# Kernel optimization log

Hardware: AMD Instinct MI355X
Metric: run time of the kernel (lower is better)

The kernel has to match this reference:

```python
import jax, jax.numpy as jnp
import numpy as np

B, C, T, F = 4, 2, 4224, 256
L = 256          # sequence_len (block size over time)
STRIDE = 128
H = 8            # num_heads
RF = L // 2      # receptive_field default


def setup_inputs() -> dict:
    key = jax.random.key(0)
    k0, k1, k2, k3, k4 = jax.random.split(key, 5)
    s = 0.05
    return {
        "x": jax.random.normal(k0, (B, C, T, F), dtype=jnp.float32),
        "w_in": jax.random.normal(k1, (3 * F, F), dtype=jnp.float32) * s,
        "b_in": jax.random.normal(k2, (3 * F,), dtype=jnp.float32) * s,
        "w_out": jax.random.normal(k3, (F, F), dtype=jnp.float32) * s,
        "b_out": jax.random.normal(k4, (F,), dtype=jnp.float32) * s,
    }


def reference(x, w_in, b_in, w_out, b_out):
    b, c, t, f = x.shape
    nb = (t - L) // STRIDE + 1              # num_blocks
    dh = f // H                              # head dim

    # --- UnfoldSpectrogram: (B,C,T,F) -> (B,C,nb,L,F) ---
    idx = jnp.arange(nb)[:, None] * STRIDE + jnp.arange(L)[None, :]  # (nb, L)
    blocks = x[:, :, idx, :]                 # (B,C,nb,L,F)

    # --- MultiheadAttention over flattened batch of blocks ---
    xb = blocks.reshape(b * c * nb, L, f)    # (N,L,F)
    qkv = xb @ w_in.T + b_in                 # (N,L,3F)
    q, k, v = jnp.split(qkv, 3, axis=-1)
    q = q.reshape(-1, L, H, dh)
    k = k.reshape(-1, L, H, dh)
    v = v.reshape(-1, L, H, dh)

    scale = 1.0 / np.sqrt(dh).astype(np.float32)
    scores = jnp.einsum("nihd,njhd->nhij", q, k) * scale  # (N,H,L,L)

    # Faithful to the original: the Longformer mask is a FLOAT 0/1 tensor that
    # torch's MultiheadAttention ADDS to the scores (band gets +1.0).
    di = jnp.arange(L)[:, None] - jnp.arange(L)[None, :]
    band = ((di >= 0) & (di < RF)).astype(scores.dtype)   # (L,L)
    scores = scores + band

    attn = jax.nn.softmax(scores, axis=-1)
    o = jnp.einsum("nhij,njhd->nihd", attn, v).reshape(-1, L, f)
    o = o @ w_out.T + b_out                  # (N,L,F)

    # --- FoldSpectrogram: overlap-add then normalize by overlap count ---
    ob = o.reshape(b, c, nb, L, f)
    y = jnp.zeros((b, c, t, f), dtype=o.dtype).at[:, :, idx, :].add(ob)
    cnt = jnp.zeros((t,), dtype=o.dtype).at[idx.reshape(-1)].add(1.0)
    return y / cnt[None, None, :, None]
```

## Files before the change

### kernel.cpp

```cpp
#include <hip/hip_runtime.h>

typedef unsigned short u16;
typedef unsigned int u32;
typedef __attribute__((ext_vector_type(8))) short bf16x8;
typedef __attribute__((ext_vector_type(4))) float f32x4;
typedef __attribute__((ext_vector_type(4))) u32 u32x4;
typedef __attribute__((ext_vector_type(2))) u32 u32x2;

__device__ __forceinline__ u16 f2bf(float f) {
  u32 u = __builtin_bit_cast(u32, f);
  return (u16)((u + 0x7FFFu + ((u >> 16) & 1u)) >> 16);
}
__device__ __forceinline__ float bf2f(u16 b) {
  return __builtin_bit_cast(float, (u32)b << 16);
}

__device__ __forceinline__ void lds_async16(const void* g, void* l) {
  auto gp = reinterpret_cast<const __attribute__((address_space(1))) u32*>(
      reinterpret_cast<uintptr_t>(g));
  auto lp = reinterpret_cast<__attribute__((address_space(3))) u32*>(
      reinterpret_cast<uintptr_t>(l));
  __builtin_amdgcn_global_load_lds(gp, lp, 16, 0, 0);
}

__global__ void cvt_kernel(const float* __restrict__ in, u16* __restrict__ out, int n4) {
  int i = blockIdx.x * 256 + threadIdx.x;
  if (i < n4) {
    f32x4 v = *(const f32x4*)(in + (size_t)i * 4);
    u32x2 o;
    o[0] = (u32)f2bf(v[0]) | ((u32)f2bf(v[1]) << 16);
    o[1] = (u32)f2bf(v[2]) | ((u32)f2bf(v[3]) << 16);
    *(u32x2*)(out + (size_t)i * 4) = o;
  }
}

template <bool OUT_BF16>
__global__ __launch_bounds__(256) void gemm_bt_kernel(
    const u16* __restrict__ A, const u16* __restrict__ B,
    const float* __restrict__ bias, void* __restrict__ C,
    int M, int N, int K) {
  __shared__ u16 sA[128 * 32];
  __shared__ u16 sB[128 * 32];
  const int tid = threadIdx.x;
  const int m0 = blockIdx.x * 128;
  const int n0 = blockIdx.y * 128;
  const int w = tid >> 6;
  const int lane = tid & 63;
  const int wr = (w >> 1) * 64;
  const int wc = (w & 1) * 64;
  const int lm = lane & 15;
  const int lk = (lane >> 4) * 8;

  f32x4 acc[4][4] = {};

  const int srow = tid >> 2;
  const int ssub = (tid & 3) * 8;
  const u16* Ag = A + (size_t)(m0 + srow) * K + ssub;
  const u16* Bg = B + (size_t)(n0 + srow) * K + ssub;
  const size_t rstep = (size_t)64 * K;

  for (int k0 = 0; k0 < K; k0 += 32) {
    __syncthreads();
    lds_async16(Ag + k0, &sA[tid * 8]);
    lds_async16(Ag + rstep + k0, &sA[2048 + tid * 8]);
    lds_async16(Bg + k0, &sB[tid * 8]);
    lds_async16(Bg + rstep + k0, &sB[2048 + tid * 8]);
    __syncthreads();
    bf16x8 af[4], bfr[4];
#pragma unroll
    for (int i = 0; i < 4; ++i)
      af[i] = *(const bf16x8*)&sA[(wr + i * 16 + lm) * 32 + lk];
#pragma unroll
    for (int j = 0; j < 4; ++j)
      bfr[j] = *(const bf16x8*)&sB[(wc + j * 16 + lm) * 32 + lk];
#pragma unroll
    for (int i = 0; i < 4; ++i)
#pragma unroll
      for (int j = 0; j < 4; ++j)
        acc[i][j] = __builtin_amdgcn_mfma_f32_16x16x32_bf16(af[i], bfr[j], acc[i][j], 0, 0, 0);
  }

  const int r0 = (lane >> 4) * 4;
#pragma unroll
  for (int j = 0; j < 4; ++j) {
    const int n = n0 + wc + j * 16 + lm;
    const float bv = bias[n];
#pragma unroll
    for (int i = 0; i < 4; ++i) {
#pragma unroll
      for (int r = 0; r < 4; ++r) {
        const int m = m0 + wr + i * 16 + r0 + r;
        float v = acc[i][j][r] + bv;
        if (OUT_BF16)
          ((u16*)C)[(size_t)m * N + n] = f2bf(v);
        else
          ((float*)C)[(size_t)m * N + n] = v;
      }
    }
  }
}

__global__ __launch_bounds__(256, 2) void attn_kernel(const u16* __restrict__ qkv,
                                                      u16* __restrict__ o_ws) {
  __shared__ u16 sK[256 * 40];
  __shared__ u16 sVt[32 * 264];
  __shared__ u16 sP[4 * 64 * 72];

  const int bid = blockIdx.x;
  const int n = bid >> 3;
  const int h = bid & 7;
  const int rowbase = (n >> 5) * 4224 + (n & 31) * 128;
  const int tid = threadIdx.x;
  const int w = tid >> 6;
  const int lane = tid & 63;
  const int lm = lane & 15;
  const int lg = lane >> 4;

#pragma unroll
  for (int it = 0; it < 4; ++it) {
    int c = it * 256 + tid;
    int row = c >> 2;
    int sub = (c & 3) * 8;
    const u16* gk = qkv + (size_t)(rowbase + row) * 768 + 256 + h * 32 + sub;
    *(u32x4*)&sK[row * 40 + sub] = *(const u32x4*)gk;
    const u16* gv = qkv + (size_t)(rowbase + row) * 768 + 512 + h * 32 + sub;
    u32x4 vv = *(const u32x4*)gv;
#pragma unroll
    for (int q = 0; q < 4; ++q) {
      sVt[(sub + 2 * q) * 264 + row] = (u16)(vv[q] & 0xFFFFu);
      sVt[(sub + 2 * q + 1) * 264 + row] = (u16)(vv[q] >> 16);
    }
  }

  bf16x8 qf[4];
#pragma unroll
  for (int rt = 0; rt < 4; ++rt) {
    int row = rowbase + w * 64 + rt * 16 + lm;
    qf[rt] = *(const bf16x8*)(qkv + (size_t)row * 768 + h * 32 + lg * 8);
  }

  __syncthreads();

  f32x4 oacc[4][2] = {};
  float lsum[4][4] = {};
  u16* myP = sP + w * (64 * 72);
  const float scale = 0.17677669529663687f;

  for (int ch = 0; ch < 4; ++ch) {
    bf16x8 kf[4];
#pragma unroll
    for (int ct = 0; ct < 4; ++ct)
      kf[ct] = *(const bf16x8*)&sK[(ch * 64 + ct * 16 + lm) * 40 + lg * 8];
    f32x4 s[4][4] = {};
#pragma unroll
    for (int rt = 0; rt < 4; ++rt)
#pragma unroll
      for (int ct = 0; ct < 4; ++ct)
        s[rt][ct] = __builtin_amdgcn_mfma_f32_16x16x32_bf16(qf[rt], kf[ct], s[rt][ct], 0, 0, 0);

#pragma unroll
    for (int rt = 0; rt < 4; ++rt)
#pragma unroll
      for (int ct = 0; ct < 4; ++ct) {
        int j = ch * 64 + ct * 16 + lm;
#pragma unroll
        for (int r = 0; r < 4; ++r) {
          int i = w * 64 + rt * 16 + lg * 4 + r;
          int di = i - j;
          float sv = s[rt][ct][r] * scale + ((di >= 0 && di < 128) ? 1.0f : 0.0f);
          float p = __expf(sv);
          lsum[rt][r] += p;
          myP[(rt * 16 + lg * 4 + r) * 72 + ct * 16 + lm] = f2bf(p);
        }
      }

#pragma unroll
    for (int kt = 0; kt < 2; ++kt) {
      bf16x8 pf[4], vf[2];
#pragma unroll
      for (int rt = 0; rt < 4; ++rt)
        pf[rt] = *(const bf16x8*)&myP[(rt * 16 + lm) * 72 + kt * 32 + lg * 8];
#pragma unroll
      for (int ct = 0; ct < 2; ++ct)
        vf[ct] = *(const bf16x8*)&sVt[(ct * 16 + lm) * 264 + ch * 64 + kt * 32 + lg * 8];
#pragma unroll
      for (int rt = 0; rt < 4; ++rt)
#pragma unroll
        for (int ct = 0; ct < 2; ++ct)
          oacc[rt][ct] = __builtin_amdgcn_mfma_f32_16x16x32_bf16(pf[rt], vf[ct], oacc[rt][ct], 0, 0, 0);
    }
  }

#pragma unroll
  for (int rt = 0; rt < 4; ++rt)
#pragma unroll
    for (int r = 0; r < 4; ++r) {
      float v = lsum[rt][r];
      v += __shfl_xor(v, 1);
      v += __shfl_xor(v, 2);
      v += __shfl_xor(v, 4);
      v += __shfl_xor(v, 8);
      lsum[rt][r] = 1.0f / v;
    }

#pragma unroll
  for (int rt = 0; rt < 4; ++rt)
#pragma unroll
    for (int ct = 0; ct < 2; ++ct)
#pragma unroll
      for (int r = 0; r < 4; ++r) {
        int i = w * 64 + rt * 16 + lg * 4 + r;
        int d = ct * 16 + lm;
        float v = oacc[rt][ct][r] * lsum[rt][r];
        o_ws[((size_t)(n * 256 + i)) * 256 + h * 32 + d] = f2bf(v);
      }
}

__global__ void combine_kernel(const u16* __restrict__ o_ws, u16* __restrict__ oc) {
  int gid = blockIdx.x * 256 + threadIdx.x;
  int m = gid >> 5;
  int f0 = (gid & 31) << 3;
  int bc = m / 4224;
  int t = m - bc * 4224;
  int i0 = t >> 7;
  float a[8] = {0.f, 0.f, 0.f, 0.f, 0.f, 0.f, 0.f, 0.f};
  if (i0 <= 31) {
    const u16* p = o_ws + ((size_t)((bc * 32 + i0) * 256 + (t - (i0 << 7)))) * 256 + f0;
    u32x4 v = *(const u32x4*)p;
#pragma unroll
    for (int q = 0; q < 4; ++q) {
      a[2 * q] += bf2f((u16)(v[q] & 0xFFFFu));
      a[2 * q + 1] += bf2f((u16)(v[q] >> 16));
    }
  }
  if (i0 >= 1) {
    int i1 = i0 - 1;
    const u16* p = o_ws + ((size_t)((bc * 32 + i1) * 256 + (t - (i1 << 7)))) * 256 + f0;
    u32x4 v = *(const u32x4*)p;
#pragma unroll
    for (int q = 0; q < 4; ++q) {
      a[2 * q] += bf2f((u16)(v[q] & 0xFFFFu));
      a[2 * q + 1] += bf2f((u16)(v[q] >> 16));
    }
  }
  float sc = (i0 >= 1 && i0 <= 31) ? 0.5f : 1.0f;
  u32x2 o;
  o[0] = (u32)f2bf(a[0] * sc) | ((u32)f2bf(a[1] * sc) << 16);
  o[1] = (u32)f2bf(a[2] * sc) | ((u32)f2bf(a[3] * sc) << 16);
  u32x2 o2;
  o2[0] = (u32)f2bf(a[4] * sc) | ((u32)f2bf(a[5] * sc) << 16);
  o2[1] = (u32)f2bf(a[6] * sc) | ((u32)f2bf(a[7] * sc) << 16);
  u16* dst = oc + (size_t)m * 256 + f0;
  *(u32x2*)dst = o;
  *(u32x2*)(dst + 4) = o2;
}

extern "C" void kernel_launch(void* const* d_in, const int* in_sizes, int n_in,
                              void* d_out, int out_size, void* d_ws, size_t ws_size,
                              hipStream_t stream) {
  const float* x = (const float*)d_in[0];
  const float* w_in = (const float*)d_in[1];
  const float* b_in = (const float*)d_in[2];
  const float* w_out = (const float*)d_in[3];
  const float* b_out = (const float*)d_in[4];
  float* y = (float*)d_out;
  char* ws = (char*)d_ws;

  u16* qkv = (u16*)(ws);
  u16* xbf = (u16*)(ws + 51904512);
  u16* ows = (u16*)(ws + 69206016);
  u16* winb = (u16*)(ws + 102760448);
  u16* woutb = (u16*)(ws + 103153664);

  cvt_kernel<<<8448, 256, 0, stream>>>(x, xbf, 2162688);
  cvt_kernel<<<192, 256, 0, stream>>>(w_in, winb, 49152);
  cvt_kernel<<<64, 256, 0, stream>>>(w_out, woutb, 16384);

  gemm_bt_kernel<true><<<dim3(264, 6), 256, 0, stream>>>(xbf, winb, b_in, qkv, 33792, 768, 256);

  attn_kernel<<<2048, 256, 0, stream>>>(qkv, ows);

  combine_kernel<<<4224, 256, 0, stream>>>(ows, xbf);

  gemm_bt_kernel<false><<<dim3(264, 2), 256, 0, stream>>>(xbf, woutb, b_out, y, 33792, 256, 256);
}
```

Before: 202.6 us.

## Restructure attention kernel: transposed scores, direct K loads, exp2 softmax, higher occupancy

Result: slower. 395.2 us (+95.1%).

```diff
diff --git a/kernel.cpp b/kernel.cpp
--- a/kernel.cpp
+++ b/kernel.cpp
@@ -13,6 +13,14 @@
 }
 __device__ __forceinline__ float bf2f(u16 b) {
   return __builtin_bit_cast(float, (u32)b << 16);
+}
+
+__device__ __forceinline__ float fexp2(float x) {
+#if __has_builtin(__builtin_amdgcn_exp2f)
+  return __builtin_amdgcn_exp2f(x);
+#else
+  return __expf(x * 0.6931471805599453f);
+#endif
 }
 
 __device__ __forceinline__ void lds_async16(const void* g, void* l) {
@@ -100,11 +108,10 @@
   }
 }
 
-__global__ __launch_bounds__(256, 2) void attn_kernel(const u16* __restrict__ qkv,
+__global__ __launch_bounds__(256, 4) void attn_kernel(const u16* __restrict__ qkv,
                                                       u16* __restrict__ o_ws) {
-  __shared__ u16 sK[256 * 40];
   __shared__ u16 sVt[32 * 264];
-  __shared__ u16 sP[4 * 64 * 72];
+  __shared__ u16 sP[4 * 64 * 40];
 
   const int bid = blockIdx.x;
   const int n = bid >> 3;
@@ -121,8 +128,6 @@
     int c = it * 256 + tid;
     int row = c >> 2;
     int sub = (c & 3) * 8;
-    const u16* gk = qkv + (size_t)(rowbase + row) * 768 + 256 + h * 32 + sub;
-    *(u32x4*)&sK[row * 40 + sub] = *(const u32x4*)gk;
     const u16* gv = qkv + (size_t)(rowbase + row) * 768 + 512 + h * 32 + sub;
     u32x4 vv = *(const u32x4*)gv;
 #pragma unroll
@@ -142,78 +147,103 @@
   __syncthreads();
 
   f32x4 oacc[4][2] = {};
-  float lsum[4][4] = {};
-  u16* myP = sP + w * (64 * 72);
-  const float scale = 0.17677669529663687f;
-
-  for (int ch = 0; ch < 4; ++ch) {
-    bf16x8 kf[4];
-#pragma unroll
-    for (int ct = 0; ct < 4; ++ct)
-      kf[ct] = *(const bf16x8*)&sK[(ch * 64 + ct * 16 + lm) * 40 + lg * 8];
-    f32x4 s[4][4] = {};
+  float lsum[4] = {0.f, 0.f, 0.f, 0.f};
+  u16* myP = sP + w * (64 * 40);
+  const float C1 = 0.25500035370494726f;
+  const float C2 = 1.4426950408889634f;
+  const int jq = lg * 4;
+
+  for (int ch = 0; ch < 8; ++ch) {
+    bf16x8 kf[2];
+#pragma unroll
+    for (int ct = 0; ct < 2; ++ct)
+      kf[ct] = *(const bf16x8*)(qkv +
+          (size_t)(rowbase + ch * 32 + ct * 16 + lm) * 768 + 256 + h * 32 + lg * 8);
+
+    f32x4 st[2][4] = {};
+#pragma unroll
+    for (int ct = 0; ct < 2; ++ct)
+#pragma unroll
+      for (int rt = 0; rt < 4; ++rt)
+        st[ct][rt] = __builtin_amdgcn_mfma_f32_16x16x32_bf16(kf[ct], qf[rt], st[ct][rt], 0, 0, 0);
+
+#pragma unroll
+    for (int ct = 0; ct < 2; ++ct) {
+#pragma unroll
+      for (int rt = 0; rt < 4; ++rt) {
+        const int D0 = w * 64 + rt * 16 - (ch * 32 + ct * 16);
+        f32x4 s = st[ct][rt];
+        float p0, p1, p2, p3;
+        if (D0 >= 16 && D0 <= 112) {
+          p0 = fexp2(__builtin_fmaf(s[0], C1, C2));
+          p1 = fexp2(__builtin_fmaf(s[1], C1, C2));
+          p2 = fexp2(__builtin_fmaf(s[2], C1, C2));
+          p3 = fexp2(__builtin_fmaf(s[3], C1, C2));
+        } else if (D0 == 0) {
+          p0 = fexp2(__builtin_fmaf(s[0], C1, (lm >= jq + 0) ? C2 : 0.0f));
+          p1 = fexp2(__builtin_fmaf(s[1], C1, (lm >= jq + 1) ? C2 : 0.0f));
+          p2 = fexp2(__builtin_fmaf(s[2], C1, (lm >= jq + 2) ? C2 : 0.0f));
+          p3 = fexp2(__builtin_fmaf(s[3], C1, (lm >= jq + 3) ? C2 : 0.0f));
+        } else if (D0 == 128) {
+          p0 = fexp2(__builtin_fmaf(s[0], C1, (lm < jq + 0) ? C2 : 0.0f));
+          p1 = fexp2(__builtin_fmaf(s[1], C1, (lm < jq + 1) ? C2 : 0.0f));
+          p2 = fexp2(__builtin_fmaf(s[2], C1, (lm < jq + 2) ? C2 : 0.0f));
+          p3 = fexp2(__builtin_fmaf(s[3], C1, (lm < jq + 3) ? C2 : 0.0f));
+        } else {
+          p0 = fexp2(s[0] * C1);
+          p1 = fexp2(s[1] * C1);
+          p2 = fexp2(s[2] * C1);
+          p3 = fexp2(s[3] * C1);
+        }
+        lsum[rt] += (p0 + p1) + (p2 + p3);
+        u32 u0 = __builtin_bit_cast(u32, p0) + 0x8000u;
+        u32 u1 = __builtin_bit_cast(u32, p1) + 0x8000u;
+        u32 u2 = __builtin_bit_cast(u32, p2) + 0x8000u;
+        u32 u3 = __builtin_bit_cast(u32, p3) + 0x8000u;
+        u32x2 pk;
+        pk[0] = __builtin_amdgcn_perm(u1, u0, 0x07060302u);
+        pk[1] = __builtin_amdgcn_perm(u3, u2, 0x07060302u);
+        *(u32x2*)&myP[(rt * 16 + lm) * 40 + ct * 16 + jq] = pk;
+      }
+    }
+
+    bf16x8 pf[4], vf[2];
 #pragma unroll
     for (int rt = 0; rt < 4; ++rt)
-#pragma unroll
-      for (int ct = 0; ct < 4; ++ct)
-        s[rt][ct] = __builtin_amdgcn_mfma_f32_16x16x32_bf16(qf[rt], kf[ct], s[rt][ct], 0, 0, 0);
-
+      pf[rt] = *(const bf16x8*)&myP[(rt * 16 + lm) * 40 + lg * 8];
+#pragma unroll
+    for (int ctd = 0; ctd < 2; ++ctd)
+      vf[ctd] = *(const bf16x8*)&sVt[(ctd * 16 + lm) * 264 + ch * 32 + lg * 8];
 #pragma unroll
     for (int rt = 0; rt < 4; ++rt)
 #pragma unroll
-      for (int ct = 0; ct < 4; ++ct) {
-        int j = ch * 64 + ct * 16 + lm;
-#pragma unroll
-        for (int r = 0; r < 4; ++r) {
-          int i = w * 64 + rt * 16 + lg * 4 + r;
-          int di = i - j;
-          float sv = s[rt][ct][r] * scale + ((di >= 0 && di < 128) ? 1.0f : 0.0f);
-          float p = __expf(sv);
-          lsum[rt][r] += p;
-          myP[(rt * 16 + lg * 4 + r) * 72 + ct * 16 + lm] = f2bf(p);
-        }
+      for (int ctd = 0; ctd < 2; ++ctd)
+        oacc[rt][ctd] = __builtin_amdgcn_mfma_f32_16x16x32_bf16(pf[rt], vf[ctd], oacc[rt][ctd], 0, 0, 0);
+  }
+
+  float linv[4];
+#pragma unroll
+  for (int rt = 0; rt < 4; ++rt) {
+    float v = lsum[rt];
+    v += __shfl_xor(v, 16);
+    v += __shfl_xor(v, 32);
+    linv[rt] = 1.0f / v;
+  }
+
+#pragma unroll
+  for (int rt = 0; rt < 4; ++rt) {
+#pragma unroll
+    for (int r = 0; r < 4; ++r) {
+      float inv = __shfl(linv[rt], jq + r);
+      int i_g = w * 64 + rt * 16 + jq + r;
+#pragma unroll
+      for (int ctd = 0; ctd < 2; ++ctd) {
+        float v = oacc[rt][ctd][r] * inv;
+        u32 u = __builtin_bit_cast(u32, v) + 0x8000u;
+        o_ws[((size_t)(n * 256 + i_g)) * 256 + h * 32 + ctd * 16 + lm] = (u16)(u >> 16);
       }
-
-#pragma unroll
-    for (int kt = 0; kt < 2; ++kt) {
-      bf16x8 pf[4], vf[2];
-#pragma unroll
-      for (int rt = 0; rt < 4; ++rt)
-        pf[rt] = *(const bf16x8*)&myP[(rt * 16 + lm) * 72 + kt * 32 + lg * 8];
-#pragma unroll
-      for (int ct = 0; ct < 2; ++ct)
-        vf[ct] = *(const bf16x8*)&sVt[(ct * 16 + lm) * 264 + ch * 64 + kt * 32 + lg * 8];
-#pragma unroll
-      for (int rt = 0; rt < 4; ++rt)
-#pragma unroll
-        for (int ct = 0; ct < 2; ++ct)
-          oacc[rt][ct] = __builtin_amdgcn_mfma_f32_16x16x32_bf16(pf[rt], vf[ct], oacc[rt][ct], 0, 0, 0);
-    }
-  }
-
-#pragma unroll
-  for (int rt = 0; rt < 4; ++rt)
-#pragma unroll
-    for (int r = 0; r < 4; ++r) {
-      float v = lsum[rt][r];
-      v += __shfl_xor(v, 1);
-      v += __shfl_xor(v, 2);
-      v += __shfl_xor(v, 4);
-      v += __shfl_xor(v, 8);
-      lsum[rt][r] = 1.0f / v;
-    }
-
-#pragma unroll
-  for (int rt = 0; rt < 4; ++rt)
-#pragma unroll
-    for (int ct = 0; ct < 2; ++ct)
-#pragma unroll
-      for (int r = 0; r < 4; ++r) {
-        int i = w * 64 + rt * 16 + lg * 4 + r;
-        int d = ct * 16 + lm;
-        float v = oacc[rt][ct][r] * lsum[rt][r];
-        o_ws[((size_t)(n * 256 + i)) * 256 + h * 32 + d] = f2bf(v);
-      }
+    }
+  }
 }
 
 __global__ void combine_kernel(const u16* __restrict__ o_ws, u16* __restrict__ oc) {
```
